# Kernel tuning notes

Measured on AMD Instinct MI355X. Metric: run time of the kernel, lower is better.

Reference implementation:

```python
import jax, jax.numpy as jnp
import numpy as np
import math

B, S, DIM, HEADS, HEAD_DIM = 2, 2048, 1024, 16, 64
ROT_DIM, ROPE_THETA = 64, 10000.0


def make_rope(seq_len):
    # DitRotary.forward: theta over half rotary_dim, duplicated interleaved pairs
    theta = 1.0 / (ROPE_THETA ** (np.arange(0, ROT_DIM, 2, dtype=np.float32) / ROT_DIM))
    pos = np.arange(seq_len, dtype=np.float32).reshape(-1, 1)
    idx = pos * theta  # [S, 32]
    cos = np.stack((np.cos(idx), np.cos(idx)), axis=-1).reshape(seq_len, -1)  # [S, 64]
    sin = np.stack((np.sin(idx), np.sin(idx)), axis=-1).reshape(seq_len, -1)
    # unsqueeze(2).unsqueeze(1) -> [1, S, 1, 64]
    return jnp.asarray(cos)[None, :, None, :], jnp.asarray(sin)[None, :, None, :]


def rotate_half(x):
    # interleaved-pair rotation: (x1, x2) -> (-x2, x1)
    x = x.reshape(*x.shape[:-1], -1, 2)
    x1, x2 = x[..., 0], x[..., 1]
    return jnp.stack((-x2, x1), axis=-1).reshape(*x.shape[:-2], -1)


def apply_rotary(x, cos, sin):
    return x * cos + rotate_half(x) * sin


def setup_inputs() -> dict:
    key = jax.random.key(0)
    ks = jax.random.split(key, 8)
    sc = 1.0 / math.sqrt(DIM)
    x = jax.random.normal(ks[0], (B, S, DIM), dtype=jnp.float32)
    cos, sin = make_rope(S)
    Wq = jax.random.normal(ks[1], (DIM, DIM), dtype=jnp.float32) * sc
    bq = jnp.zeros((DIM,), jnp.float32)
    Wk = jax.random.normal(ks[2], (DIM, DIM), dtype=jnp.float32) * sc
    bk = jnp.zeros((DIM,), jnp.float32)
    Wv = jax.random.normal(ks[3], (DIM, DIM), dtype=jnp.float32) * sc
    bv = jnp.zeros((DIM,), jnp.float32)
    Wo = jax.random.normal(ks[4], (DIM, DIM), dtype=jnp.float32) * sc
    bo = jnp.zeros((DIM,), jnp.float32)
    mask = jnp.ones((B, 1, 1, S), dtype=bool)
    return {"x": x, "cos": cos, "sin": sin, "Wq": Wq, "bq": bq, "Wk": Wk,
            "bk": bk, "Wv": Wv, "bv": bv, "Wo": Wo, "bo": bo, "mask": mask}


def reference(x, cos, sin, Wq, bq, Wk, bk, Wv, bv, Wo, bo, mask):
    b, s, _ = x.shape
    q = (x @ Wq.T + bq).reshape(b, s, HEADS, HEAD_DIM)
    k = (x @ Wk.T + bk).reshape(b, s, HEADS, HEAD_DIM)
    v = (x @ Wv.T + bv).reshape(b, s, HEADS, HEAD_DIM)
    # partial rotary: applied only to head index 0 (dim 2 of [B,S,H,D])
    q = jnp.concatenate([apply_rotary(q[:, :, :1, :], cos, sin), q[:, :, 1:, :]], axis=2)
    k = jnp.concatenate([apply_rotary(k[:, :, :1, :], cos, sin), k[:, :, 1:, :]], axis=2)
    # [B,H,S,D]
    q = q.transpose(0, 2, 1, 3)
    k = k.transpose(0, 2, 1, 3)
    v = v.transpose(0, 2, 1, 3)
    neg = jnp.finfo(jnp.float32).min
    attn_mask = jnp.where(mask, 0.0, neg)  # ~mask * finfo.min
    scores = jnp.einsum("bhsd,bhtd->bhst", q, k) / math.sqrt(HEAD_DIM)
    scores = scores + attn_mask
    probs = jax.nn.softmax(scores.astype(jnp.float32), axis=-1).astype(q.dtype)
    out = jnp.einsum("bhst,bhtd->bhsd", probs, v)
    out = out.transpose(0, 2, 1, 3).reshape(b, s, HEADS * HEAD_DIM)
    return out @ Wo.T + bo
```

## Files before the change

kernel.cpp:

```cpp
#include <hip/hip_runtime.h>
#include <hip/hip_bf16.h>


typedef __attribute__((ext_vector_type(8))) __bf16 bf16x8;
typedef __attribute__((ext_vector_type(4))) __bf16 bf16x4;
typedef __attribute__((ext_vector_type(4))) float f32x4;
typedef __attribute__((ext_vector_type(4))) short s16x4;

#define NB_B 2
#define NB_S 2048
#define NB_DIM 1024
#define NB_H 16
#define NB_HD 64
#define NB_BS (NB_B * NB_S)

__device__ __forceinline__ void async_cp16(const __bf16* g, __bf16* l) {
    __builtin_amdgcn_global_load_lds(
        (const __attribute__((address_space(1))) unsigned int*)g,
        (__attribute__((address_space(3))) unsigned int*)l, 16, 0, 0);
}

__global__ __launch_bounds__(256) void cvt_kernel(
    const float* __restrict__ x,  const float* __restrict__ wq,
    const float* __restrict__ wk, const float* __restrict__ wv,
    const float* __restrict__ wo,
    __bf16* __restrict__ xb,  __bf16* __restrict__ wqb,
    __bf16* __restrict__ wkb, __bf16* __restrict__ wvb,
    __bf16* __restrict__ wob) {
    const int XQ = (NB_BS * NB_DIM) / 4;
    const int WQ = (NB_DIM * NB_DIM) / 4;
    int i = blockIdx.x * 256 + threadIdx.x;
    const float* src; __bf16* dst; int off;
    if (i < XQ)              { src = x;  dst = xb;  off = i; }
    else if (i < XQ + WQ)    { src = wq; dst = wqb; off = i - XQ; }
    else if (i < XQ + 2*WQ)  { src = wk; dst = wkb; off = i - XQ - WQ; }
    else if (i < XQ + 3*WQ)  { src = wv; dst = wvb; off = i - XQ - 2*WQ; }
    else                     { src = wo; dst = wob; off = i - XQ - 3*WQ; }
    f32x4 v = *(const f32x4*)(src + (size_t)off * 4);
    bf16x4 b;
#pragma unroll
    for (int j = 0; j < 4; ++j) b[j] = (__bf16)v[j];
    *(bf16x4*)(dst + (size_t)off * 4) = b;
}

__global__ __launch_bounds__(256) void gemm_qkv_kernel(
    const __bf16* __restrict__ A,
    const float* __restrict__ cosb, const float* __restrict__ sinb,
    const __bf16* __restrict__ Wq, const float* __restrict__ bq, __bf16* __restrict__ qbuf,
    const __bf16* __restrict__ Wk, const float* __restrict__ bk, __bf16* __restrict__ kbuf,
    const __bf16* __restrict__ Wv, const float* __restrict__ bv, __bf16* __restrict__ vtbuf) {
    constexpr int K = 1024;
    constexpr int NT = K / 32;
    __shared__ __align__(16) __bf16 As[3][128][32];
    __shared__ __align__(16) __bf16 Bs[3][128][32];

    const int z = blockIdx.z;
    const __bf16* W; const float* bias;
    if (z == 0)      { W = Wq; bias = bq; }
    else if (z == 1) { W = Wk; bias = bk; }
    else             { W = Wv; bias = bv; }

    const int tid = threadIdx.x;
    const int lane = tid & 63;
    const int w = tid >> 6;
    const int wm = w >> 1, wn = w & 1;
    const int row16 = lane & 15, quad = lane >> 4;
    const int m0 = blockIdx.x * 128, n0 = blockIdx.y * 128;

    f32x4 acc[4][4] = {};

    auto stage = [&](int nb, int kt) {
#pragma unroll
        for (int i = 0; i < 2; ++i) {
            int c = tid + i * 256;
            int row = c >> 2;
            int co = (c & 3) << 3;
            async_cp16(A + (size_t)(m0 + row) * K + kt + co, &As[nb][row][co]);
            async_cp16(W + (size_t)(n0 + row) * K + kt + co, &Bs[nb][row][co]);
        }
    };
    auto compute = [&](int nb) {
        bf16x8 af[4], bfr[4];
#pragma unroll
        for (int t = 0; t < 4; ++t) {
            af[t]  = *(const bf16x8*)&As[nb][wm * 64 + t * 16 + row16][quad * 8];
            bfr[t] = *(const bf16x8*)&Bs[nb][wn * 64 + t * 16 + row16][quad * 8];
        }
        __builtin_amdgcn_s_setprio(1);
#pragma unroll
        for (int mt = 0; mt < 4; ++mt)
#pragma unroll
            for (int nt = 0; nt < 4; ++nt)
                acc[mt][nt] = __builtin_amdgcn_mfma_f32_16x16x32_bf16(af[mt], bfr[nt], acc[mt][nt], 0, 0, 0);
        __builtin_amdgcn_s_setprio(0);
    };

    stage(0, 0);
    stage(1, 32);
    int cu = 0, pfb = 2;
    for (int t = 0; t < NT - 1; ++t) {
        asm volatile("s_waitcnt vmcnt(4)" ::: "memory");
        __builtin_amdgcn_s_barrier();
        if (t + 2 < NT) stage(pfb, (t + 2) * 32);
        compute(cu);
        cu  = (cu  == 2) ? 0 : cu + 1;
        pfb = (pfb == 2) ? 0 : pfb + 1;
    }
    asm volatile("s_waitcnt vmcnt(0)" ::: "memory");
    __builtin_amdgcn_s_barrier();
    compute(cu);

    if (z == 2) {
#pragma unroll
        for (int mt = 0; mt < 4; ++mt) {
            int row = m0 + wm * 64 + mt * 16 + quad * 4;
            int b = row >> 11, s = row & (NB_S - 1);
#pragma unroll
            for (int nt = 0; nt < 4; ++nt) {
                int col = n0 + wn * 64 + nt * 16 + row16;
                float bv = bias[col];
                bf16x4 pack;
#pragma unroll
                for (int r = 0; r < 4; ++r) pack[r] = (__bf16)(acc[mt][nt][r] + bv);
                *(bf16x4*)&vtbuf[(size_t)b * (NB_DIM * NB_S) + (size_t)col * NB_S + s] = pack;
            }
        }
    } else {
        __bf16* C = (z == 0) ? qbuf : kbuf;
        const bool rope = (n0 == 0) && (wn == 0);
#pragma unroll
        for (int mt = 0; mt < 4; ++mt) {
            int row = m0 + wm * 64 + mt * 16 + quad * 4;
#pragma unroll
            for (int nt = 0; nt < 4; ++nt) {
                int col = n0 + wn * 64 + nt * 16 + row16;
                float bv = bias[col];
#pragma unroll
                for (int r = 0; r < 4; ++r) {
                    float val = acc[mt][nt][r] + bv;
                    if (rope) {
                        float part = __shfl_xor(val, 1, 64);
                        int srow = (row + r) & (NB_S - 1);
                        float c  = cosb[srow * 64 + col];
                        float sn = sinb[srow * 64 + col];
                        val = (lane & 1) ? (val * c + part * sn) : (val * c - part * sn);
                    }
                    C[(size_t)(row + r) * NB_DIM + col] = (__bf16)val;
                }
            }
        }
    }
}

__global__ __launch_bounds__(256) void gemm_o_kernel(
    const __bf16* __restrict__ A, const __bf16* __restrict__ W,
    const float* __restrict__ bias, float* __restrict__ C) {
    constexpr int K = 1024;
    constexpr int NT = K / 32;
    __shared__ __align__(16) __bf16 As[3][128][32];
    __shared__ __align__(16) __bf16 Bs[3][64][32];

    const int tid = threadIdx.x;
    const int lane = tid & 63;
    const int w = tid >> 6;
    const int row16 = lane & 15, quad = lane >> 4;
    const int m0 = blockIdx.x * 128, n0 = blockIdx.y * 64;

    f32x4 acc[2][4] = {};

    auto stage = [&](int nb, int kt) {
#pragma unroll
        for (int i = 0; i < 2; ++i) {
            int c = tid + i * 256;
            int row = c >> 2;
            int co = (c & 3) << 3;
            async_cp16(A + (size_t)(m0 + row) * K + kt + co, &As[nb][row][co]);
        }
        {
            int row = tid >> 2;
            int co = (tid & 3) << 3;
            async_cp16(W + (size_t)(n0 + row) * K + kt + co, &Bs[nb][row][co]);
        }
    };
    auto compute = [&](int nb) {
        bf16x8 af[2], bfr[4];
#pragma unroll
        for (int t = 0; t < 2; ++t)
            af[t] = *(const bf16x8*)&As[nb][w * 32 + t * 16 + row16][quad * 8];
#pragma unroll
        for (int nt = 0; nt < 4; ++nt)
            bfr[nt] = *(const bf16x8*)&Bs[nb][nt * 16 + row16][quad * 8];
        __builtin_amdgcn_s_setprio(1);
#pragma unroll
        for (int mt = 0; mt < 2; ++mt)
#pragma unroll
            for (int nt = 0; nt < 4; ++nt)
                acc[mt][nt] = __builtin_amdgcn_mfma_f32_16x16x32_bf16(af[mt], bfr[nt], acc[mt][nt], 0, 0, 0);
        __builtin_amdgcn_s_setprio(0);
    };

    stage(0, 0);
    stage(1, 32);
    int cu = 0, pfb = 2;
    for (int t = 0; t < NT - 1; ++t) {
        asm volatile("s_waitcnt vmcnt(3)" ::: "memory");
        __builtin_amdgcn_s_barrier();
        if (t + 2 < NT) stage(pfb, (t + 2) * 32);
        compute(cu);
        cu  = (cu  == 2) ? 0 : cu + 1;
        pfb = (pfb == 2) ? 0 : pfb + 1;
    }
    asm volatile("s_waitcnt vmcnt(0)" ::: "memory");
    __builtin_amdgcn_s_barrier();
    compute(cu);

#pragma unroll
    for (int mt = 0; mt < 2; ++mt) {
        int row = m0 + w * 32 + mt * 16 + quad * 4;
#pragma unroll
        for (int nt = 0; nt < 4; ++nt) {
            int col = n0 + nt * 16 + row16;
            float bv = bias[col];
#pragma unroll
            for (int r = 0; r < 4; ++r)
                C[(size_t)(row + r) * NB_DIM + col] = acc[mt][nt][r] + bv;
        }
    }
}

__global__ __launch_bounds__(256) void attn_kernel(const __bf16* __restrict__ qb,
                                                   const __bf16* __restrict__ kb,
                                                   const __bf16* __restrict__ vtb,
                                                   __bf16* __restrict__ ob) {
    __shared__ __align__(16) __bf16 Ks[128][72];
    __shared__ __align__(16) __bf16 Vts[64][132];

    const int tid = threadIdx.x;
    const int lane = tid & 63;
    const int w = tid >> 6;
    const int row16 = lane & 15, quad = lane >> 4;
    const int bh = blockIdx.y;
    const int b = bh >> 4, h = bh & 15;
    const int q0 = blockIdx.x * 128 + w * 32;

    const size_t headoff = (size_t)b * NB_S * NB_DIM + (size_t)h * NB_HD;
    const size_t vtoff = (size_t)b * (NB_DIM * NB_S) + (size_t)(h * NB_HD) * NB_S;

    const float qscale = 0.18033688011112042f;
    bf16x8 qf[2][2];
#pragma unroll
    for (int m = 0; m < 2; ++m)
#pragma unroll
        for (int hh = 0; hh < 2; ++hh) {
            bf16x8 v = *(const bf16x8*)(qb + headoff + (size_t)(q0 + m * 16 + row16) * NB_DIM + hh * 32 + quad * 8);
#pragma unroll
            for (int j = 0; j < 8; ++j) v[j] = (__bf16)((float)v[j] * qscale);
            qf[m][hh] = v;
        }

    f32x4 o[2][4] = {};
    f32x4 ol[2] = {};

    const short one_bf16 = (short)0x3F80;
    const s16x4 onesf = {one_bf16, one_bf16, one_bf16, one_bf16};

    bf16x8 kreg[4], vreg[4];
#pragma unroll
    for (int i = 0; i < 4; ++i) {
        int c = tid + i * 256;
        kreg[i] = *(const bf16x8*)(kb + headoff + (size_t)(c >> 3) * NB_DIM + ((c & 7) << 3));
        vreg[i] = *(const bf16x8*)(vtb + vtoff + (size_t)(c >> 4) * NB_S + ((c & 15) << 3));
    }

    for (int kt = 0; kt < 16; ++kt) {
        __syncthreads();
#pragma unroll
        for (int i = 0; i < 4; ++i) {
            int c = tid + i * 256;
            *(bf16x8*)&Ks[c >> 3][(c & 7) << 3] = kreg[i];
            bf16x4 lo, hi;
#pragma unroll
            for (int j = 0; j < 4; ++j) { lo[j] = vreg[i][j]; hi[j] = vreg[i][j + 4]; }
            *(bf16x4*)&Vts[c >> 4][(c & 15) << 3] = lo;
            *(bf16x4*)&Vts[c >> 4][((c & 15) << 3) + 4] = hi;
        }
        __syncthreads();
        if (kt < 15) {
            int base = (kt + 1) * 128;
#pragma unroll
            for (int i = 0; i < 4; ++i) {
                int c = tid + i * 256;
                kreg[i] = *(const bf16x8*)(kb + headoff + (size_t)(base + (c >> 3)) * NB_DIM + ((c & 7) << 3));
                vreg[i] = *(const bf16x8*)(vtb + vtoff + (size_t)(c >> 4) * NB_S + base + ((c & 15) << 3));
            }
        }

        s16x4 pf[2][8];
#pragma unroll
        for (int t = 0; t < 8; ++t) {
            f32x4 s0 = {}, s1 = {};
            __builtin_amdgcn_s_setprio(1);
#pragma unroll
            for (int hh = 0; hh < 2; ++hh) {
                bf16x8 kf = *(const bf16x8*)&Ks[t * 16 + row16][hh * 32 + quad * 8];
                s0 = __builtin_amdgcn_mfma_f32_16x16x32_bf16(kf, qf[0][hh], s0, 0, 0, 0);
                s1 = __builtin_amdgcn_mfma_f32_16x16x32_bf16(kf, qf[1][hh], s1, 0, 0, 0);
            }
            __builtin_amdgcn_s_setprio(0);
            bf16x4 p0, p1;
#pragma unroll
            for (int r = 0; r < 4; ++r) {
                float e0 = __builtin_amdgcn_exp2f(s0[r]); p0[r] = (__bf16)e0;
                float e1 = __builtin_amdgcn_exp2f(s1[r]); p1[r] = (__bf16)e1;
            }
            pf[0][t] = __builtin_bit_cast(s16x4, p0);
            pf[1][t] = __builtin_bit_cast(s16x4, p1);
            ol[0] = __builtin_amdgcn_mfma_f32_16x16x16bf16_1k(pf[0][t], onesf, ol[0], 0, 0, 0);
            ol[1] = __builtin_amdgcn_mfma_f32_16x16x16bf16_1k(pf[1][t], onesf, ol[1], 0, 0, 0);
        }

        __builtin_amdgcn_s_setprio(1);
#pragma unroll
        for (int nt = 0; nt < 4; ++nt)
#pragma unroll
            for (int t = 0; t < 8; ++t) {
                s16x4 vf = *(const s16x4*)&Vts[nt * 16 + row16][t * 16 + quad * 4];
                o[0][nt] = __builtin_amdgcn_mfma_f32_16x16x16bf16_1k(pf[0][t], vf, o[0][nt], 0, 0, 0);
                o[1][nt] = __builtin_amdgcn_mfma_f32_16x16x16bf16_1k(pf[1][t], vf, o[1][nt], 0, 0, 0);
            }
        __builtin_amdgcn_s_setprio(0);
    }

#pragma unroll
    for (int m = 0; m < 2; ++m)
#pragma unroll
        for (int r = 0; r < 4; ++r) {
            float inv = 1.f / ol[m][r];
            int row = q0 + m * 16 + quad * 4 + r;
#pragma unroll
            for (int nt = 0; nt < 4; ++nt)
                ob[headoff + (size_t)row * NB_DIM + nt * 16 + row16] = (__bf16)(o[m][nt][r] * inv);
        }
}

extern "C" void kernel_launch(void* const* d_in, const int* in_sizes, int n_in,
                              void* d_out, int out_size, void* d_ws, size_t ws_size,
                              hipStream_t stream) {
    const float* x    = (const float*)d_in[0];
    const float* cosb = (const float*)d_in[1];
    const float* sinb = (const float*)d_in[2];
    const float* Wq   = (const float*)d_in[3];
    const float* bq   = (const float*)d_in[4];
    const float* Wk   = (const float*)d_in[5];
    const float* bk   = (const float*)d_in[6];
    const float* Wv   = (const float*)d_in[7];
    const float* bv   = (const float*)d_in[8];
    const float* Wo   = (const float*)d_in[9];
    const float* bo   = (const float*)d_in[10];

    __bf16* qbuf  = (__bf16*)d_ws;
    __bf16* kbuf  = qbuf + (size_t)NB_BS * NB_DIM;
    __bf16* vtbuf = kbuf + (size_t)NB_BS * NB_DIM;
    __bf16* abuf  = vtbuf + (size_t)NB_BS * NB_DIM;
    __bf16* xb    = abuf + (size_t)NB_BS * NB_DIM;
    __bf16* wqb   = xb + (size_t)NB_BS * NB_DIM;
    __bf16* wkb   = wqb + (size_t)NB_DIM * NB_DIM;
    __bf16* wvb   = wkb + (size_t)NB_DIM * NB_DIM;
    __bf16* wob   = wvb + (size_t)NB_DIM * NB_DIM;

    const int XQ = (NB_BS * NB_DIM) / 4, WQ = (NB_DIM * NB_DIM) / 4;
    cvt_kernel<<<(XQ + 4 * WQ) / 256, 256, 0, stream>>>(x, Wq, Wk, Wv, Wo,
                                                        xb, wqb, wkb, wvb, wob);

    dim3 gqkv(NB_BS / 128, NB_DIM / 128, 3);
    gemm_qkv_kernel<<<gqkv, 256, 0, stream>>>(xb, cosb, sinb,
                                              wqb, bq, qbuf,
                                              wkb, bk, kbuf,
                                              wvb, bv, vtbuf);

    attn_kernel<<<dim3(NB_S / 128, NB_B * NB_H), 256, 0, stream>>>(qbuf, kbuf, vtbuf, abuf);

    dim3 go(NB_BS / 128, NB_DIM / 64);
    gemm_o_kernel<<<go, 256, 0, stream>>>(abuf, wob, bo, (float*)d_out);
}
```

Before: 211.6 us.

## Rewrite QKV GEMM with 256x256 tiles, 8 waves, swizzled LDS, interleaved staging

The QKV projection GEMM now uses 256x256 output tiles with 512 threads and BK=64 double-buffered LDS. An XOR swizzle on the LDS layout is meant to avoid bank conflicts, and global loads for the next stages are interleaved with four quadrant MFMA phases. It treats Wq/Wk/Wv as one concatenated 3072-row weight matrix (relying on contiguous workspace layout) and routes the epilogue by column block. Larger tiles raise reuse per LDS byte but cut the grid to 192 blocks and raise register pressure.

After: 214.0 us. About the same (+1.1%).

```diff
diff --git a/kernel.cpp b/kernel.cpp
--- a/kernel.cpp
+++ b/kernel.cpp
@@ -43,109 +43,175 @@
     *(bf16x4*)(dst + (size_t)off * 4) = b;
 }
 
-__global__ __launch_bounds__(256) void gemm_qkv_kernel(
-    const __bf16* __restrict__ A,
+__global__ __launch_bounds__(512, 2) void gemm_qkv_kernel(
+    const __bf16* __restrict__ A, const __bf16* __restrict__ W,
     const float* __restrict__ cosb, const float* __restrict__ sinb,
-    const __bf16* __restrict__ Wq, const float* __restrict__ bq, __bf16* __restrict__ qbuf,
-    const __bf16* __restrict__ Wk, const float* __restrict__ bk, __bf16* __restrict__ kbuf,
-    const __bf16* __restrict__ Wv, const float* __restrict__ bv, __bf16* __restrict__ vtbuf) {
+    const float* __restrict__ bq, const float* __restrict__ bk, const float* __restrict__ bv,
+    __bf16* __restrict__ qbuf, __bf16* __restrict__ kbuf, __bf16* __restrict__ vtbuf) {
     constexpr int K = 1024;
-    constexpr int NT = K / 32;
-    __shared__ __align__(16) __bf16 As[3][128][32];
-    __shared__ __align__(16) __bf16 Bs[3][128][32];
-
-    const int z = blockIdx.z;
-    const __bf16* W; const float* bias;
-    if (z == 0)      { W = Wq; bias = bq; }
-    else if (z == 1) { W = Wk; bias = bk; }
-    else             { W = Wv; bias = bv; }
+    constexpr int NT = 16;
+    __shared__ __align__(16) __bf16 As[2][256][64];
+    __shared__ __align__(16) __bf16 Bs[2][256][64];
 
     const int tid = threadIdx.x;
     const int lane = tid & 63;
     const int w = tid >> 6;
-    const int wm = w >> 1, wn = w & 1;
+    const int wm = w >> 2, wn = w & 3;
     const int row16 = lane & 15, quad = lane >> 4;
-    const int m0 = blockIdx.x * 128, n0 = blockIdx.y * 128;
-
-    f32x4 acc[4][4] = {};
-
-    auto stage = [&](int nb, int kt) {
+    const int r7 = row16 & 7;
+    const int m0 = blockIdx.x * 256, n0 = blockIdx.y * 256;
+
+    auto stage_half = [&](int T, int kind) {
+        const int bi = T & 1, kb = T * 64;
 #pragma unroll
         for (int i = 0; i < 2; ++i) {
-            int c = tid + i * 256;
-            int row = c >> 2;
-            int co = (c & 3) << 3;
-            async_cp16(A + (size_t)(m0 + row) * K + kt + co, &As[nb][row][co]);
-            async_cp16(W + (size_t)(n0 + row) * K + kt + co, &Bs[nb][row][co]);
+            int si = tid + i * 512;
+            int row = si >> 3, g = si & 7;
+            int gcol = ((g ^ (row & 7)) << 3);
+            if (kind == 0)
+                async_cp16(A + (size_t)(m0 + row) * K + kb + gcol, &As[bi][row][g << 3]);
+            else if (kind == 3)
+                async_cp16(A + (size_t)(m0 + 128 + row) * K + kb + gcol, &As[bi][128 + row][g << 3]);
+            else if (kind == 1)
+                async_cp16(W + (size_t)(n0 + row) * K + kb + gcol, &Bs[bi][row][g << 3]);
+            else
+                async_cp16(W + (size_t)(n0 + 128 + row) * K + kb + gcol, &Bs[bi][128 + row][g << 3]);
         }
     };
-    auto compute = [&](int nb) {
-        bf16x8 af[4], bfr[4];
-#pragma unroll
-        for (int t = 0; t < 4; ++t) {
-            af[t]  = *(const bf16x8*)&As[nb][wm * 64 + t * 16 + row16][quad * 8];
-            bfr[t] = *(const bf16x8*)&Bs[nb][wn * 64 + t * 16 + row16][quad * 8];
-        }
-        __builtin_amdgcn_s_setprio(1);
-#pragma unroll
-        for (int mt = 0; mt < 4; ++mt)
-#pragma unroll
-            for (int nt = 0; nt < 4; ++nt)
-                acc[mt][nt] = __builtin_amdgcn_mfma_f32_16x16x32_bf16(af[mt], bfr[nt], acc[mt][nt], 0, 0, 0);
-        __builtin_amdgcn_s_setprio(0);
-    };
-
-    stage(0, 0);
-    stage(1, 32);
-    int cu = 0, pfb = 2;
-    for (int t = 0; t < NT - 1; ++t) {
-        asm volatile("s_waitcnt vmcnt(4)" ::: "memory");
-        __builtin_amdgcn_s_barrier();
-        if (t + 2 < NT) stage(pfb, (t + 2) * 32);
-        compute(cu);
-        cu  = (cu  == 2) ? 0 : cu + 1;
-        pfb = (pfb == 2) ? 0 : pfb + 1;
-    }
-    asm volatile("s_waitcnt vmcnt(0)" ::: "memory");
+
+    f32x4 acc[8][4] = {};
+    bf16x8 afr[4][2], bfr0[2][2], bfr1[2][2];
+
+    stage_half(0, 0); stage_half(0, 1); stage_half(0, 2); stage_half(0, 3);
+    stage_half(1, 0); stage_half(1, 1); stage_half(1, 2);
+    asm volatile("s_waitcnt vmcnt(6)" ::: "memory");
     __builtin_amdgcn_s_barrier();
-    compute(cu);
+
+    for (int kt = 0; kt < NT; ++kt) {
+        const int bi = kt & 1;
+
+#pragma unroll
+        for (int mi = 0; mi < 4; ++mi)
+#pragma unroll
+            for (int kk = 0; kk < 2; ++kk)
+                afr[mi][kk] = *(const bf16x8*)&As[bi][wm * 64 + mi * 16 + row16][((kk * 4 + quad) ^ r7) << 3];
+#pragma unroll
+        for (int ni = 0; ni < 2; ++ni)
+#pragma unroll
+            for (int kk = 0; kk < 2; ++kk)
+                bfr0[ni][kk] = *(const bf16x8*)&Bs[bi][wn * 32 + ni * 16 + row16][((kk * 4 + quad) ^ r7) << 3];
+        if (kt + 1 < NT) stage_half(kt + 1, 3);
+        asm volatile("s_waitcnt lgkmcnt(8)" ::: "memory");
+        __builtin_amdgcn_s_barrier();
+        asm volatile("s_waitcnt lgkmcnt(0)" ::: "memory");
+        __builtin_amdgcn_sched_barrier(0);
+        __builtin_amdgcn_s_setprio(1);
+#pragma unroll
+        for (int mi = 0; mi < 4; ++mi)
+#pragma unroll
+            for (int ni = 0; ni < 2; ++ni)
+#pragma unroll
+                for (int kk = 0; kk < 2; ++kk)
+                    acc[mi][ni] = __builtin_amdgcn_mfma_f32_16x16x32_bf16(afr[mi][kk], bfr0[ni][kk], acc[mi][ni], 0, 0, 0);
+        __builtin_amdgcn_s_setprio(0);
+        __builtin_amdgcn_s_barrier();
+
+#pragma unroll
+        for (int ni = 0; ni < 2; ++ni)
+#pragma unroll
+            for (int kk = 0; kk < 2; ++kk)
+                bfr1[ni][kk] = *(const bf16x8*)&Bs[bi][128 + wn * 32 + ni * 16 + row16][((kk * 4 + quad) ^ r7) << 3];
+        if (kt + 2 < NT) stage_half(kt + 2, 0);
+        __builtin_amdgcn_s_barrier();
+        asm volatile("s_waitcnt lgkmcnt(0)" ::: "memory");
+        __builtin_amdgcn_sched_barrier(0);
+        __builtin_amdgcn_s_setprio(1);
+#pragma unroll
+        for (int mi = 0; mi < 4; ++mi)
+#pragma unroll
+            for (int ni = 0; ni < 2; ++ni)
+#pragma unroll
+                for (int kk = 0; kk < 2; ++kk)
+                    acc[mi][2 + ni] = __builtin_amdgcn_mfma_f32_16x16x32_bf16(afr[mi][kk], bfr1[ni][kk], acc[mi][2 + ni], 0, 0, 0);
+        __builtin_amdgcn_s_setprio(0);
+        __builtin_amdgcn_s_barrier();
+
+#pragma unroll
+        for (int mi = 0; mi < 4; ++mi)
+#pragma unroll
+            for (int kk = 0; kk < 2; ++kk)
+                afr[mi][kk] = *(const bf16x8*)&As[bi][128 + wm * 64 + mi * 16 + row16][((kk * 4 + quad) ^ r7) << 3];
+        if (kt + 2 < NT) stage_half(kt + 2, 1);
+        __builtin_amdgcn_s_barrier();
+        asm volatile("s_waitcnt lgkmcnt(0)" ::: "memory");
+        __builtin_amdgcn_sched_barrier(0);
+        __builtin_amdgcn_s_setprio(1);
+#pragma unroll
+        for (int mi = 0; mi < 4; ++mi)
+#pragma unroll
+            for (int ni = 0; ni < 2; ++ni)
+#pragma unroll
+                for (int kk = 0; kk < 2; ++kk)
+                    acc[4 + mi][2 + ni] = __builtin_amdgcn_mfma_f32_16x16x32_bf16(afr[mi][kk], bfr1[ni][kk], acc[4 + mi][2 + ni], 0, 0, 0);
+        __builtin_amdgcn_s_setprio(0);
+        __builtin_amdgcn_s_barrier();
+
+        if (kt + 2 < NT) stage_half(kt + 2, 2);
+        __builtin_amdgcn_s_barrier();
+        __builtin_amdgcn_s_setprio(1);
+#pragma unroll
+        for (int mi = 0; mi < 4; ++mi)
+#pragma unroll
+            for (int ni = 0; ni < 2; ++ni)
+#pragma unroll
+                for (int kk = 0; kk < 2; ++kk)
+                    acc[4 + mi][ni] = __builtin_amdgcn_mfma_f32_16x16x32_bf16(afr[mi][kk], bfr0[ni][kk], acc[4 + mi][ni], 0, 0, 0);
+        __builtin_amdgcn_s_setprio(0);
+        if (kt < NT - 2)       { asm volatile("s_waitcnt vmcnt(6)" ::: "memory"); __builtin_amdgcn_s_barrier(); }
+        else if (kt == NT - 2) { asm volatile("s_waitcnt vmcnt(0)" ::: "memory"); __builtin_amdgcn_s_barrier(); }
+    }
+
+    const int z = n0 >> 10;
+    const int n0l = n0 & 1023;
+    const float* bias = (z == 0) ? bq : (z == 1) ? bk : bv;
 
     if (z == 2) {
 #pragma unroll
-        for (int mt = 0; mt < 4; ++mt) {
-            int row = m0 + wm * 64 + mt * 16 + quad * 4;
-            int b = row >> 11, s = row & (NB_S - 1);
-#pragma unroll
-            for (int nt = 0; nt < 4; ++nt) {
-                int col = n0 + wn * 64 + nt * 16 + row16;
-                float bv = bias[col];
+        for (int mi = 0; mi < 8; ++mi) {
+            int grow = m0 + (mi >> 2) * 128 + wm * 64 + (mi & 3) * 16 + quad * 4;
+            int bb = grow >> 11, s = grow & (NB_S - 1);
+#pragma unroll
+            for (int ni = 0; ni < 4; ++ni) {
+                int col = n0l + (ni >> 1) * 128 + wn * 32 + (ni & 1) * 16 + row16;
+                float bvv = bias[col];
                 bf16x4 pack;
 #pragma unroll
-                for (int r = 0; r < 4; ++r) pack[r] = (__bf16)(acc[mt][nt][r] + bv);
-                *(bf16x4*)&vtbuf[(size_t)b * (NB_DIM * NB_S) + (size_t)col * NB_S + s] = pack;
+                for (int r = 0; r < 4; ++r) pack[r] = (__bf16)(acc[mi][ni][r] + bvv);
+                *(bf16x4*)&vtbuf[(size_t)bb * (NB_DIM * NB_S) + (size_t)col * NB_S + s] = pack;
             }
         }
     } else {
         __bf16* C = (z == 0) ? qbuf : kbuf;
-        const bool rope = (n0 == 0) && (wn == 0);
-#pragma unroll
-        for (int mt = 0; mt < 4; ++mt) {
-            int row = m0 + wm * 64 + mt * 16 + quad * 4;
-#pragma unroll
-            for (int nt = 0; nt < 4; ++nt) {
-                int col = n0 + wn * 64 + nt * 16 + row16;
-                float bv = bias[col];
+        const bool ropew = (n0l == 0) && (wn < 2);
+#pragma unroll
+        for (int mi = 0; mi < 8; ++mi) {
+            int grow = m0 + (mi >> 2) * 128 + wm * 64 + (mi & 3) * 16 + quad * 4;
+#pragma unroll
+            for (int ni = 0; ni < 4; ++ni) {
+                int col = n0l + (ni >> 1) * 128 + wn * 32 + (ni & 1) * 16 + row16;
+                float bvv = bias[col];
+                const bool rope = ropew && (ni < 2);
 #pragma unroll
                 for (int r = 0; r < 4; ++r) {
-                    float val = acc[mt][nt][r] + bv;
+                    float val = acc[mi][ni][r] + bvv;
                     if (rope) {
                         float part = __shfl_xor(val, 1, 64);
-                        int srow = (row + r) & (NB_S - 1);
+                        int srow = (grow + r) & (NB_S - 1);
                         float c  = cosb[srow * 64 + col];
                         float sn = sinb[srow * 64 + col];
                         val = (lane & 1) ? (val * c + part * sn) : (val * c - part * sn);
                     }
-                    C[(size_t)(row + r) * NB_DIM + col] = (__bf16)val;
+                    C[(size_t)(grow + r) * NB_DIM + col] = (__bf16)val;
                 }
             }
         }
@@ -372,11 +438,9 @@
     cvt_kernel<<<(XQ + 4 * WQ) / 256, 256, 0, stream>>>(x, Wq, Wk, Wv, Wo,
                                                         xb, wqb, wkb, wvb, wob);
 
-    dim3 gqkv(NB_BS / 128, NB_DIM / 128, 3);
-    gemm_qkv_kernel<<<gqkv, 256, 0, stream>>>(xb, cosb, sinb,
-                                              wqb, bq, qbuf,
-                                              wkb, bk, kbuf,
-                                              wvb, bv, vtbuf);
+    dim3 gqkv(NB_BS / 256, (3 * NB_DIM) / 256);
+    gemm_qkv_kernel<<<gqkv, 512, 0, stream>>>(xb, wqb, cosb, sinb,
+                                              bq, bk, bv, qbuf, kbuf, vtbuf);
 
     attn_kernel<<<dim3(NB_S / 128, NB_B * NB_H), 256, 0, stream>>>(qbuf, kbuf, vtbuf, abuf);
 
```
